# Performance work log

Hardware: AMD Instinct MI355X
Metric: run time of the kernel (lower is better)

## Reference

```python
import jax, jax.numpy as jnp
import numpy as np

C = 128      # channels
IN_A = 1024  # audio feature dim
IN_V = 512   # video feature dim
N = 20000    # nodes
E = 120000   # edges
NA = 10000   # number of audio nodes (placed first)
EPS = 1e-5


def _bn(h, p):
    # eval-mode BatchNorm1d: p = [gamma, beta, running_mean, running_var], each [F]
    return (h - p[2]) * jax.lax.rsqrt(p[3] + EPS) * p[0] + p[1]


def _lpp(h, bn1, W1, bn2, W2):
    # LinearPathPreact: BN -> ReLU -> Linear(no bias) -> BN -> ReLU -> Linear(no bias)
    h = jax.nn.relu(_bn(h, bn1)) @ W1.T
    h = jax.nn.relu(_bn(h, bn2)) @ W2.T
    return h


def _edge_conv(feats, src, dst, active, bn1, W1, bn2, W2, n_nodes):
    # PyG EdgeConv, aggr='max': out_i = max_{j->i} nn([x_i, x_j - x_i])
    xi = feats[dst]                      # [E, C] target features
    xj = feats[src]                      # [E, C] source features
    msg = _lpp(jnp.concatenate([xi, xj - xi], axis=-1), bn1, W1, bn2, W2)  # [E, C]
    neg = jnp.finfo(msg.dtype).min
    msg = jnp.where(active[:, None], msg, neg)  # mask out inactive edges for max
    agg = jax.ops.segment_max(msg, dst, num_segments=n_nodes)  # [N, C]
    return jnp.where(agg <= neg, jnp.zeros((), agg.dtype), agg)  # isolated nodes -> 0


def setup_inputs() -> dict:
    key = jax.random.key(0)
    ks = jax.random.split(key, 24)

    def bn_params(k, f, lead=()):
        kk = jax.random.split(k, 4)
        g = 1.0 + 0.1 * jax.random.normal(kk[0], lead + (f,), jnp.float32)
        b = 0.1 * jax.random.normal(kk[1], lead + (f,), jnp.float32)
        m = 0.1 * jax.random.normal(kk[2], lead + (f,), jnp.float32)
        v = 0.5 + jax.random.uniform(kk[3], lead + (f,), jnp.float32)
        return jnp.stack([g, b, m, v], axis=-2)  # lead + [4, f]

    inp = {}
    inp['x'] = jax.random.normal(ks[0], (N, 2, IN_A), jnp.float32)
    inp['edge_index'] = jax.random.randint(ks[1], (2, E), 0, N, dtype=jnp.int32)
    inp['edge_delta'] = jax.random.randint(ks[2], (E,), 0, 8, dtype=jnp.int32)
    inp['edge_self'] = jax.random.randint(ks[3], (E,), 0, 2, dtype=jnp.int32)
    inp['n_audio'] = NA

    s_a = (2.0 / IN_A) ** 0.5
    s_v = (2.0 / IN_V) ** 0.5
    s_2c = (2.0 / (2 * C)) ** 0.5
    s_c = (2.0 / C) ** 0.5
    inp['w0a'] = s_a * jax.random.normal(ks[4], (C, IN_A), jnp.float32)
    inp['b0a'] = 0.01 * jax.random.normal(ks[5], (C,), jnp.float32)
    inp['w0v'] = s_v * jax.random.normal(ks[6], (C, IN_V), jnp.float32)
    inp['b0v'] = 0.01 * jax.random.normal(ks[7], (C,), jnp.float32)
    inp['bn0'] = bn_params(ks[8], C)
    inp['bn_node'] = bn_params(ks[9], C, lead=(3,))          # batch_1..3: [3,4,C]
    # 8 EdgeConv MLPs in order [l1, l1t, l2, l2t, l3, l3t, l4, l4t]
    inp['ec_bn1'] = bn_params(ks[10], 2 * C, lead=(8,))      # [8,4,2C]
    inp['ec_fc1'] = s_2c * jax.random.normal(ks[11], (8, C, 2 * C), jnp.float32)
    inp['ec_bn2'] = bn_params(ks[12], C, lead=(8,))          # [8,4,C]
    inp['ec_fc2'] = s_c * jax.random.normal(ks[13], (8, C, C), jnp.float32)
    # heads: [fc, fc_a, fc_v]
    inp['w_heads'] = s_c * jax.random.normal(ks[14], (3, 2, C), jnp.float32)
    inp['b_heads'] = 0.01 * jax.random.normal(ks[15], (3, 2), jnp.float32)
    return inp


def reference(x, edge_index, edge_delta, edge_self, n_audio,
              w0a, b0a, w0v, b0v, bn0, bn_node,
              ec_bn1, ec_fc1, ec_bn2, ec_fc2, w_heads, b_heads):
    n = x.shape[0]
    src, dst = edge_index[0], edge_index[1]
    active1 = edge_delta < 1
    active2 = ((edge_delta >= 1) & (edge_delta < 4)) | (edge_self == 1)

    # layer 0: audio nodes are the first n_audio nodes (static split)
    a = x[:n_audio, 0, :IN_A] @ w0a.T + b0a          # [NA, C]
    v = x[n_audio:, 1, :IN_V] @ w0v.T + b0v          # [N-NA, C]
    g0 = jax.nn.relu(_bn(jnp.concatenate([a, v], axis=0), bn0))  # [N, C]

    def ec(f, k, act):
        return _edge_conv(f, src, dst, act, ec_bn1[k], ec_fc1[k], ec_bn2[k], ec_fc2[k], n)

    g1 = ec(ec(g0, 0, active1), 1, active2)
    g1 = jax.nn.relu(_bn(g1, bn_node[0]))            # dropout is identity (eval)
    g2 = ec(ec(g1, 2, active1), 3, active2) + g1
    g2 = jax.nn.relu(_bn(g2, bn_node[1]))
    g3 = ec(ec(g2, 4, active1), 5, active2) + g2
    g3 = jax.nn.relu(_bn(g3, bn_node[2]))
    g4 = ec(ec(g3, 6, active1), 7, active2) + g3

    out = g4 @ w_heads[0].T + b_heads[0]             # [N, 2]
    audio_out = g0[:n_audio] @ w_heads[1].T + b_heads[1]  # [NA, 2]
    video_out = g0[n_audio:] @ w_heads[2].T + b_heads[2]  # [N-NA, 2]
    return out, audio_out, video_out
```

## Files before the change

### kernel.cpp

```cpp
#include <hip/hip_runtime.h>

#define C 128
#define IN_A 1024
#define IN_V 512
#define NNODE 20000
#define NE 120000
#define NA 10000
#define NV 10000
#define EPSBN 1e-5f
#define NPAD 20032
#define EPAD 120064
#define NSTRIDE 20032

typedef __bf16 bf16_t;
typedef bf16_t bf16x8 __attribute__((ext_vector_type(8)));
typedef bf16_t bf16x2 __attribute__((ext_vector_type(2)));
typedef float f32x4 __attribute__((ext_vector_type(4)));
typedef unsigned int u32;

__device__ __forceinline__ f32x4 ld4(const float* p) {
    return *reinterpret_cast<const f32x4*>(p);
}
__device__ __forceinline__ f32x4 ld4nt(const float* p) {
    return __builtin_nontemporal_load(reinterpret_cast<const f32x4*>(p));
}
__device__ __forceinline__ int xcd_swz(int b, int n) {
    int q = n >> 3, r = n & 7;
    int x = b & 7, i = b >> 3;
    return (x < r ? x * (q + 1) : r * (q + 1) + (x - r) * q) + i;
}

struct PB {
    const float* x;
    const int* esrc; const int* edst; const int* edelta; const int* eself;
    const float* b0a; const float* b0v;
    const float* w0a; const float* w0v;
    const float* bn0; const float* bnn;
    const float* ecb1; const float* ecf1; const float* ecb2; const float* ecf2;
    const float* wh; const float* bh;
    float* out;
    bf16_t* W16; float* SBN; int* cnts; int* indeg; int* rowst; int* curs;
    int* psrc; int* pdst;
    float* U; bf16_t* G0; bf16_t* G1; bf16_t* msg;
};

__global__ void prep0(PB P) {
    int b = blockIdx.x, t = threadIdx.x;
    if (b < 2304) {
        int i = b * 256 + t;
        float v;
        if (i < 131072) v = P.w0a[i];
        else if (i < 196608) v = P.w0v[i - 131072];
        else if (i < 458752) v = P.ecf1[i - 196608];
        else v = P.ecf2[i - 458752];
        P.W16[i] = (bf16_t)v;
    } else if (b < 2318) {
        int i = (b - 2304) * 256 + t;
        if (i >= 28 * 128) return;
        int pair = i >> 7, cc = i & 127;
        float gg, bb, mm, vv;
        if (pair == 0)      { gg = P.bn0[cc]; bb = P.bn0[128 + cc]; mm = P.bn0[256 + cc]; vv = P.bn0[384 + cc]; }
        else if (pair < 4)  { const float* q = P.bnn + (pair - 1) * 512;
                              gg = q[cc]; bb = q[128 + cc]; mm = q[256 + cc]; vv = q[384 + cc]; }
        else if (pair < 12) { const float* q = P.ecb1 + (pair - 4) * 1024;
                              gg = q[cc]; bb = q[256 + cc]; mm = q[512 + cc]; vv = q[768 + cc]; }
        else if (pair < 20) { const float* q = P.ecb1 + (pair - 12) * 1024 + 128;
                              gg = q[cc]; bb = q[256 + cc]; mm = q[512 + cc]; vv = q[768 + cc]; }
        else                { const float* q = P.ecb2 + (pair - 20) * 512;
                              gg = q[cc]; bb = q[128 + cc]; mm = q[256 + cc]; vv = q[384 + cc]; }
        float sv = gg * rsqrtf(vv + EPSBN);
        P.SBN[pair * 256 + cc] = sv;
        P.SBN[pair * 256 + 128 + cc] = bb - mm * sv;
    } else {
        int e = (b - 2318) * 256 + t;
        if (e >= NE) return;
        int d = P.edelta[e];
        int dn = P.edst[e];
        if (d < 1) atomicAdd(P.indeg + dn, 1);
        if (((d >= 1) && (d < 4)) || (P.eself[e] == 1)) atomicAdd(P.indeg + NSTRIDE + dn, 1);
    }
}

__global__ __launch_bounds__(1024) void scan_kernel(PB P) {
    __shared__ int sh[1024];
    int half = blockIdx.x;
    const int* in = P.indeg + half * NSTRIDE;
    int* rsw = P.rowst + half * NSTRIDE;
    int* cu = P.curs + half * NSTRIDE;
    int t = threadIdx.x;
    int base = t * 20;
    int s = 0;
    for (int i = 0; i < 20; i++) { int idx = base + i; if (idx < NNODE) s += in[idx]; }
    sh[t] = s;
    __syncthreads();
    for (int off = 1; off < 1024; off <<= 1) {
        int v = (t >= off) ? sh[t - off] : 0;
        __syncthreads();
        sh[t] += v;
        __syncthreads();
    }
    int run = sh[t] - s;
    for (int i = 0; i < 20; i++) {
        int idx = base + i;
        if (idx < NNODE) { int v = in[idx]; rsw[idx] = run; cu[idx] = run; run += v; }
    }
    if (t == 1023) { rsw[NNODE] = sh[1023]; P.cnts[half] = sh[1023]; }
}

__global__ __launch_bounds__(256) void combo0(PB P) {
    __shared__ __align__(16) char smem[16384];
    int b = blockIdx.x;
    if (b >= 314) {
        int e = (b - 314) * 256 + threadIdx.x;
        if (e >= NE) return;
        int d = P.edelta[e];
        int dn = P.edst[e], sn = P.esrc[e];
        if (d < 1) {
            int q = atomicAdd(P.curs + dn, 1);
            P.psrc[q] = sn; P.pdst[q] = dn;
        }
        if (((d >= 1) && (d < 4)) || (P.eself[e] == 1)) {
            int q = atomicAdd(P.curs + NSTRIDE + dn, 1);
            P.psrc[EPAD + q] = sn; P.pdst[EPAD + q] = dn;
        }
        return;
    }
    int wave = threadIdx.x >> 6, lane = threadIdx.x & 63;
    bool audio = b < 157;
    int tile = audio ? b : b - 157;
    const float* A = audio ? P.x : P.x + (size_t)NA * 2048 + 1024;
    const bf16_t* W = audio ? P.W16 : P.W16 + 131072;
    const float* bias = audio ? P.b0a : P.b0v;
    int K = audio ? IN_A : IN_V;
    int M = audio ? NA : NV;
    int nbase = audio ? 0 : NA;
    int hsel = audio ? 1 : 2;

    int m0 = tile * 64 + wave * 16;
    int arow = m0 + (lane & 15);
    int ar = arow < M ? arow : (M - 1);
    int ak = (lane >> 4) << 3;
    const float* Af = A + (size_t)ar * 2048 + ak;
    const bf16_t* Bp = W + (size_t)(lane & 15) * K + ak;

    f32x4 acc[8];
#pragma unroll
    for (int i = 0; i < 8; i++) acc[i] = (f32x4)(0.0f);
    for (int kk = 0; kk < K; kk += 32) {
        f32x4 v0 = ld4nt(Af + kk), v1 = ld4nt(Af + kk + 4);
        bf16x8 a;
#pragma unroll
        for (int j = 0; j < 4; j++) { a[j] = (bf16_t)v0[j]; a[4 + j] = (bf16_t)v1[j]; }
#pragma unroll
        for (int nt = 0; nt < 8; nt++) {
            bf16x8 bb = *reinterpret_cast<const bf16x8*>(Bp + (size_t)nt * 16 * K + kk);
            acc[nt] = __builtin_amdgcn_mfma_f32_16x16x32_bf16(a, bb, acc[nt], 0, 0, 0);
        }
    }
    int cb = lane & 15;
    float se[8], he[8], bs[8], w0[8], w1[8], s1[8], t1[8];
#pragma unroll
    for (int nt = 0; nt < 8; nt++) {
        int n = nt * 16 + cb;
        se[nt] = P.SBN[n]; he[nt] = P.SBN[128 + n]; bs[nt] = bias[n];
        w0[nt] = P.wh[hsel * 256 + n]; w1[nt] = P.wh[hsel * 256 + 128 + n];
        s1[nt] = P.SBN[4 * 256 + n]; t1[nt] = P.SBN[4 * 256 + 128 + n];
    }
    int rbase = (lane >> 4) * 4;
#pragma unroll
    for (int j = 0; j < 4; j++) {
        int m = m0 + rbase + j;
        int r = wave * 16 + rbase + j;
        float hp0 = 0.f, hp1 = 0.f;
#pragma unroll
        for (int nt = 0; nt < 8; nt++) {
            int n = nt * 16 + cb;
            float v = fmaxf((acc[nt][j] + bs[nt]) * se[nt] + he[nt], 0.0f);
            if (m < M) P.G0[(size_t)(nbase + m) * C + n] = (bf16_t)v;
            hp0 += v * w0[nt]; hp1 += v * w1[nt];
            float av = fmaxf(v * s1[nt] + t1[nt], 0.0f);
            int byte = (r * 256 + 2 * n) ^ ((r & 7) << 4);
            *reinterpret_cast<bf16_t*>(smem + byte) = (bf16_t)av;
        }
#pragma unroll
        for (int o = 8; o; o >>= 1) { hp0 += __shfl_xor(hp0, o); hp1 += __shfl_xor(hp1, o); }
        if (cb == 0 && m < M) {
            float* op = audio ? (P.out + 40000 + (size_t)m * 2)
                              : (P.out + 60000 + (size_t)m * 2);
            op[0] = hp0 + P.bh[hsel * 2 + 0];
            op[1] = hp1 + P.bh[hsel * 2 + 1];
        }
    }
    const bf16_t* B2p = P.W16 + 196608 + (size_t)(lane & 15) * 256 + ak;
#pragma unroll
    for (int i = 0; i < 8; i++) acc[i] = (f32x4)(0.0f);
    int rr = wave * 16 + (lane & 15);
#pragma unroll
    for (int kk = 0; kk < C; kk += 32) {
        int byte = (rr * 256 + 2 * (ak + kk)) ^ ((rr & 7) << 4);
        bf16x8 a = *reinterpret_cast<const bf16x8*>(smem + byte);
#pragma unroll
        for (int nt = 0; nt < 8; nt++) {
            bf16x8 bb = *reinterpret_cast<const bf16x8*>(B2p + (size_t)nt * 16 * 256 + kk);
            acc[nt] = __builtin_amdgcn_mfma_f32_16x16x32_bf16(a, bb, acc[nt], 0, 0, 0);
        }
    }
#pragma unroll
    for (int j = 0; j < 4; j++) {
        int m = m0 + rbase + j;
        if (m >= M) continue;
#pragma unroll
        for (int nt = 0; nt < 8; nt++)
            P.U[(size_t)(nbase + m) * C + nt * 16 + cb] = acc[nt][j];
    }
}

__global__ __launch_bounds__(256) void edge_k(PB P, int h) {
    __shared__ __align__(16) float hlds[4 * 2048];
    int half = h & 1;
    int Mreal = P.cnts[half];
    int tiles = (Mreal + 63) >> 6;
    if ((int)blockIdx.x >= tiles) return;
    int m0b = xcd_swz(blockIdx.x, tiles) * 64;
    const bf16_t* F = half ? P.G1 : P.G0;
    const int* psrc = P.psrc + (half ? EPAD : 0);
    const int* pdst = P.pdst + (half ? EPAD : 0);
    const bf16_t* B1 = P.W16 + 196608 + (size_t)h * 32768 + 128;
    const bf16_t* B2 = P.W16 + 458752 + (size_t)h * 16384;
    const float* sA = P.SBN + (12 + h) * 256; const float* shA = sA + 128;
    const float* sE = P.SBN + (20 + h) * 256; const float* shE = sE + 128;

    int wave = threadIdx.x >> 6;
    int lane = threadIdx.x & 63;
    int m0 = m0b + wave * 16;
    int arow = m0 + (lane & 15);
    int ar = arow < Mreal ? arow : (Mreal - 1);
    int ak = (lane >> 4) << 3;

    const bf16_t* Fs = F + (size_t)psrc[ar] * C + ak;
    const bf16_t* Fd = F + (size_t)pdst[ar] * C + ak;
    const bf16_t* B1p = B1 + (size_t)(lane & 15) * 256 + ak;

    f32x4 acc[8];
#pragma unroll
    for (int i = 0; i < 8; i++) acc[i] = (f32x4)(0.0f);
#pragma unroll
    for (int kk = 0; kk < C; kk += 32) {
        bf16x8 s8 = *reinterpret_cast<const bf16x8*>(Fs + kk);
        bf16x8 d8 = *reinterpret_cast<const bf16x8*>(Fd + kk);
        f32x4 s0 = ld4(sA + kk + ak), s1 = ld4(sA + kk + ak + 4);
        f32x4 h0 = ld4(shA + kk + ak), h1 = ld4(shA + kk + ak + 4);
        bf16x8 a;
#pragma unroll
        for (int j = 0; j < 4; j++) {
            float t0 = fmaxf(((float)s8[j] - (float)d8[j]) * s0[j] + h0[j], 0.0f);
            float t1 = fmaxf(((float)s8[4 + j] - (float)d8[4 + j]) * s1[j] + h1[j], 0.0f);
            a[j] = (bf16_t)t0; a[4 + j] = (bf16_t)t1;
        }
#pragma unroll
        for (int nt = 0; nt < 8; nt++) {
            bf16x8 bb = *reinterpret_cast<const bf16x8*>(B1p + (size_t)nt * 16 * 256 + kk);
            acc[nt] = __builtin_amdgcn_mfma_f32_16x16x32_bf16(a, bb, acc[nt], 0, 0, 0);
        }
    }
    int cb = lane & 15;
    float se[8], he[8];
#pragma unroll
    for (int nt = 0; nt < 8; nt++) { se[nt] = sE[nt * 16 + cb]; he[nt] = shE[nt * 16 + cb]; }
    int rbase = (lane >> 4) * 4;
    float* wl = hlds + wave * 2048;
#pragma unroll
    for (int j = 0; j < 4; j++) {
        int m = m0 + rbase + j;
        int mc = m < Mreal ? m : (Mreal - 1);
        const float* Ur = P.U + (size_t)pdst[mc] * C;
        int r = rbase + j;
        int sw = (r & 7) << 2;
#pragma unroll
        for (int nt = 0; nt < 8; nt++) {
            int n = nt * 16 + cb;
            float v = acc[nt][j] + Ur[n];
            wl[(r * 128 + n) ^ sw] = fmaxf(v * se[nt] + he[nt], 0.0f);
        }
    }
    const bf16_t* B2p = B2 + (size_t)(lane & 15) * C + ak;
#pragma unroll
    for (int i = 0; i < 8; i++) acc[i] = (f32x4)(0.0f);
    int rr = lane & 15;
    int swz = (rr & 7) << 2;
    const float* rl = hlds + wave * 2048;
#pragma unroll
    for (int kk = 0; kk < C; kk += 32) {
        int c0 = kk + ak;
        f32x4 v0 = *reinterpret_cast<const f32x4*>(rl + ((rr * 128 + c0) ^ swz));
        f32x4 v1 = *reinterpret_cast<const f32x4*>(rl + ((rr * 128 + c0 + 4) ^ swz));
        bf16x8 a;
#pragma unroll
        for (int j = 0; j < 4; j++) { a[j] = (bf16_t)v0[j]; a[4 + j] = (bf16_t)v1[j]; }
#pragma unroll
        for (int nt = 0; nt < 8; nt++) {
            bf16x8 bb = *reinterpret_cast<const bf16x8*>(B2p + (size_t)nt * 16 * C + kk);
            acc[nt] = __builtin_amdgcn_mfma_f32_16x16x32_bf16(a, bb, acc[nt], 0, 0, 0);
        }
    }
#pragma unroll
    for (int j = 0; j < 4; j++) {
        int m = m0 + rbase + j;
        if (m < Mreal) {
            bf16_t* op = P.msg + (size_t)m * C;
#pragma unroll
            for (int nt = 0; nt < 8; nt++) op[nt * 16 + cb] = (bf16_t)acc[nt][j];
        }
    }
}

__global__ __launch_bounds__(512) void aggk1(PB P, int h) {
    __shared__ __align__(16) char smem[4096];
    int half = h & 1, p = h >> 1;
    int tile = xcd_swz(blockIdx.x, 1250);
    int wave = threadIdx.x >> 6;
    int lane = threadIdx.x & 63;
    const int* rs = P.rowst + half * NSTRIDE;
    const u32* msgu = (const u32*)P.msg;
    int c = lane * 2;

    const float* s1a = P.SBN + (5 + h) * 256;
    float s1c0 = s1a[c], s1c1 = s1a[c + 1], h1c0 = s1a[128 + c], h1c1 = s1a[128 + c + 1];
    float sn0 = 0.f, sn1 = 0.f, hn0 = 0.f, hn1 = 0.f;
    if (half && p < 3) {
        const float* q = P.SBN + (1 + p) * 256;
        sn0 = q[c]; sn1 = q[c + 1]; hn0 = q[128 + c]; hn1 = q[128 + c + 1];
    }
    float w0c0 = 0.f, w0c1 = 0.f, w1c0 = 0.f, w1c1 = 0.f;
    if (h == 7) { w0c0 = P.wh[c]; w0c1 = P.wh[c + 1]; w1c0 = P.wh[128 + c]; w1c1 = P.wh[129 + c]; }

#pragma unroll
    for (int i = 0; i < 2; i++) {
        int n = tile * 16 + wave * 2 + i;
        int r = wave * 2 + i;
        float a0 = 0.f, a1 = 0.f;
        if (n < NNODE) {
            int p0 = rs[n], p1 = rs[n + 1];
            float v0 = -INFINITY, v1 = -INFINITY;
            int q = p0;
            for (; q + 1 < p1; q += 2) {
                u32 u0 = msgu[(size_t)q * 64 + lane];
                u32 u1 = msgu[(size_t)(q + 1) * 64 + lane];
                v0 = fmaxf(v0, __uint_as_float(u0 << 16));
                v1 = fmaxf(v1, __uint_as_float(u0 & 0xffff0000u));
                v0 = fmaxf(v0, __uint_as_float(u1 << 16));
                v1 = fmaxf(v1, __uint_as_float(u1 & 0xffff0000u));
            }
            if (q < p1) {
                u32 u = msgu[(size_t)q * 64 + lane];
                v0 = fmaxf(v0, __uint_as_float(u << 16));
                v1 = fmaxf(v1, __uint_as_float(u & 0xffff0000u));
            }
            if (p1 == p0) { v0 = 0.f; v1 = 0.f; }
            if (h == 7) {
                bf16x2 r2 = *((const bf16x2*)(P.G0 + (size_t)n * C) + lane);
                v0 += (float)r2[0]; v1 += (float)r2[1];
                float q0 = v0 * w0c0 + v1 * w0c1;
                float q1 = v0 * w1c0 + v1 * w1c1;
#pragma unroll
                for (int o = 32; o; o >>= 1) { q0 += __shfl_down(q0, o); q1 += __shfl_down(q1, o); }
                if (lane == 0) {
                    P.out[(size_t)n * 2 + 0] = q0 + P.bh[0];
                    P.out[(size_t)n * 2 + 1] = q1 + P.bh[1];
                }
            } else {
                float g0v, g1v;
                if (!half) {
                    g0v = v0; g1v = v1;
                    bf16x2 w; w[0] = (bf16_t)g0v; w[1] = (bf16_t)g1v;
                    *((bf16x2*)(P.G1 + (size_t)n * C) + lane) = w;
                } else {
                    float r0 = 0.f, r1 = 0.f;
                    if (p >= 1) {
                        bf16x2 r2 = *((const bf16x2*)(P.G0 + (size_t)n * C) + lane);
                        r0 = (float)r2[0]; r1 = (float)r2[1];
                    }
                    g0v = fmaxf((v0 + r0) * sn0 + hn0, 0.0f);
                    g1v = fmaxf((v1 + r1) * sn1 + hn1, 0.0f);
                    bf16x2 w; w[0] = (bf16_t)g0v; w[1] = (bf16_t)g1v;
                    *((bf16x2*)(P.G0 + (size_t)n * C) + lane) = w;
                }
                a0 = fmaxf(g0v * s1c0 + h1c0, 0.0f);
                a1 = fmaxf(g1v * s1c1 + h1c1, 0.0f);
            }
        }
        if (h < 7) {
            int byte = (r * 256 + lane * 4) ^ ((r & 7) << 4);
            bf16x2 t; t[0] = (bf16_t)a0; t[1] = (bf16_t)a1;
            *reinterpret_cast<bf16x2*>(smem + byte) = t;
        }
    }
    if (h == 7) return;
    __syncthreads();
    const bf16_t* B = P.W16 + 196608 + (size_t)(h + 1) * 32768;
    int cb = lane & 15;
    int ak = (lane >> 4) << 3;
    const bf16_t* Bp = B + (size_t)(wave * 16 + cb) * 256 + ak;
    f32x4 acc = (f32x4)(0.0f);
#pragma unroll
    for (int kk = 0; kk < C; kk += 32) {
        int byte = (cb * 256 + 2 * (ak + kk)) ^ ((cb & 7) << 4);
        bf16x8 a = *reinterpret_cast<const bf16x8*>(smem + byte);
        bf16x8 bb = *reinterpret_cast<const bf16x8*>(Bp + kk);
        acc = __builtin_amdgcn_mfma_f32_16x16x32_bf16(a, bb, acc, 0, 0, 0);
    }
#pragma unroll
    for (int j = 0; j < 4; j++) {
        int m = tile * 16 + (lane >> 4) * 4 + j;
        if (m < NNODE) P.U[(size_t)m * C + wave * 16 + cb] = acc[j];
    }
}

extern "C" void kernel_launch(void* const* d_in, const int* in_sizes, int n_in,
                              void* d_out, int out_size, void* d_ws, size_t ws_size,
                              hipStream_t stream) {
    PB P;
    P.x      = (const float*)d_in[0];
    const int* eidx = (const int*)d_in[1];
    P.esrc   = eidx;
    P.edst   = eidx + NE;
    P.edelta = (const int*)d_in[2];
    P.eself  = (const int*)d_in[3];
    P.w0a    = (const float*)d_in[5];
    P.b0a    = (const float*)d_in[6];
    P.w0v    = (const float*)d_in[7];
    P.b0v    = (const float*)d_in[8];
    P.bn0    = (const float*)d_in[9];
    P.bnn    = (const float*)d_in[10];
    P.ecb1   = (const float*)d_in[11];
    P.ecf1   = (const float*)d_in[12];
    P.ecb2   = (const float*)d_in[13];
    P.ecf2   = (const float*)d_in[14];
    P.wh     = (const float*)d_in[15];
    P.bh     = (const float*)d_in[16];
    P.out    = (float*)d_out;

    char* wsb = (char*)d_ws;
    size_t off = 0;
    auto take = [&](size_t bytes) -> char* {
        char* p = wsb + off;
        off = (off + bytes + 255) & ~(size_t)255;
        return p;
    };
    P.W16   = (bf16_t*)take(589824 * 2);
    P.SBN   = (float*)take(28 * 256 * 4);
    P.cnts  = (int*)take(256);
    P.indeg = (int*)take(2 * NSTRIDE * 4);
    P.rowst = (int*)take((2 * NSTRIDE + 64) * 4);
    P.curs  = (int*)take(2 * NSTRIDE * 4);
    P.psrc  = (int*)take(2 * (size_t)EPAD * 4);
    P.pdst  = (int*)take(2 * (size_t)EPAD * 4);
    P.U     = (float*)take((size_t)NPAD * C * 4);
    P.G0    = (bf16_t*)take((size_t)NPAD * C * 2);
    P.G1    = (bf16_t*)take((size_t)NPAD * C * 2);
    P.msg   = (bf16_t*)take((size_t)EPAD * C * 2);
    (void)ws_size; (void)in_sizes; (void)n_in; (void)out_size;

    hipMemsetAsync(P.indeg, 0, 2 * NSTRIDE * 4, stream);
    prep0<<<2787, 256, 0, stream>>>(P);
    scan_kernel<<<2, 1024, 0, stream>>>(P);
    combo0<<<783, 256, 0, stream>>>(P);
    for (int h = 0; h < 8; h++) {
        edge_k<<<EPAD / 64, 256, 0, stream>>>(P, h);
        aggk1<<<1250, 512, 0, stream>>>(P, h);
    }
}
```

Measured before the change: 524.2 us.

## Compute x_i half of first EdgeConv linear per edge instead of precomputed node table

Removes the per-node precomputation U = W1a·relu(bn(x_i)) that combo0 and aggk1 produced, along with its fp32 workspace buffer. Instead edge_k now runs a full K=256 MFMA per edge: the destination-feature half (BN and ReLU on x_i) and the difference half (x_j - x_i). This drops the per-node GEMMs and the random fp32 U gathers per edge, at the cost of doubling the first-layer MFMA work in the edge kernel. It also adds an occupancy hint of 4 blocks per CU on edge_k.

```diff
diff --git a/kernel.cpp b/kernel.cpp
--- a/kernel.cpp
+++ b/kernel.cpp
@@ -41,7 +41,7 @@
     float* out;
     bf16_t* W16; float* SBN; int* cnts; int* indeg; int* rowst; int* curs;
     int* psrc; int* pdst;
-    float* U; bf16_t* G0; bf16_t* G1; bf16_t* msg;
+    bf16_t* G0; bf16_t* G1; bf16_t* msg;
 };
 
 __global__ void prep0(PB P) {
@@ -108,7 +108,6 @@
 }
 
 __global__ __launch_bounds__(256) void combo0(PB P) {
-    __shared__ __align__(16) char smem[16384];
     int b = blockIdx.x;
     if (b >= 314) {
         int e = (b - 314) * 256 + threadIdx.x;
@@ -158,19 +157,17 @@
         }
     }
     int cb = lane & 15;
-    float se[8], he[8], bs[8], w0[8], w1[8], s1[8], t1[8];
+    float se[8], he[8], bs[8], w0[8], w1[8];
 #pragma unroll
     for (int nt = 0; nt < 8; nt++) {
         int n = nt * 16 + cb;
         se[nt] = P.SBN[n]; he[nt] = P.SBN[128 + n]; bs[nt] = bias[n];
         w0[nt] = P.wh[hsel * 256 + n]; w1[nt] = P.wh[hsel * 256 + 128 + n];
-        s1[nt] = P.SBN[4 * 256 + n]; t1[nt] = P.SBN[4 * 256 + 128 + n];
     }
     int rbase = (lane >> 4) * 4;
 #pragma unroll
     for (int j = 0; j < 4; j++) {
         int m = m0 + rbase + j;
-        int r = wave * 16 + rbase + j;
         float hp0 = 0.f, hp1 = 0.f;
 #pragma unroll
         for (int nt = 0; nt < 8; nt++) {
@@ -178,9 +175,6 @@
             float v = fmaxf((acc[nt][j] + bs[nt]) * se[nt] + he[nt], 0.0f);
             if (m < M) P.G0[(size_t)(nbase + m) * C + n] = (bf16_t)v;
             hp0 += v * w0[nt]; hp1 += v * w1[nt];
-            float av = fmaxf(v * s1[nt] + t1[nt], 0.0f);
-            int byte = (r * 256 + 2 * n) ^ ((r & 7) << 4);
-            *reinterpret_cast<bf16_t*>(smem + byte) = (bf16_t)av;
         }
 #pragma unroll
         for (int o = 8; o; o >>= 1) { hp0 += __shfl_xor(hp0, o); hp1 += __shfl_xor(hp1, o); }
@@ -191,31 +185,9 @@
             op[1] = hp1 + P.bh[hsel * 2 + 1];
         }
     }
-    const bf16_t* B2p = P.W16 + 196608 + (size_t)(lane & 15) * 256 + ak;
-#pragma unroll
-    for (int i = 0; i < 8; i++) acc[i] = (f32x4)(0.0f);
-    int rr = wave * 16 + (lane & 15);
-#pragma unroll
-    for (int kk = 0; kk < C; kk += 32) {
-        int byte = (rr * 256 + 2 * (ak + kk)) ^ ((rr & 7) << 4);
-        bf16x8 a = *reinterpret_cast<const bf16x8*>(smem + byte);
-#pragma unroll
-        for (int nt = 0; nt < 8; nt++) {
-            bf16x8 bb = *reinterpret_cast<const bf16x8*>(B2p + (size_t)nt * 16 * 256 + kk);
-            acc[nt] = __builtin_amdgcn_mfma_f32_16x16x32_bf16(a, bb, acc[nt], 0, 0, 0);
-        }
-    }
-#pragma unroll
-    for (int j = 0; j < 4; j++) {
-        int m = m0 + rbase + j;
-        if (m >= M) continue;
-#pragma unroll
-        for (int nt = 0; nt < 8; nt++)
-            P.U[(size_t)(nbase + m) * C + nt * 16 + cb] = acc[nt][j];
-    }
-}
-
-__global__ __launch_bounds__(256) void edge_k(PB P, int h) {
+}
+
+__global__ __launch_bounds__(256, 4) void edge_k(PB P, int h) {
     __shared__ __align__(16) float hlds[4 * 2048];
     int half = h & 1;
     int Mreal = P.cnts[half];
@@ -225,9 +197,10 @@
     const bf16_t* F = half ? P.G1 : P.G0;
     const int* psrc = P.psrc + (half ? EPAD : 0);
     const int* pdst = P.pdst + (half ? EPAD : 0);
-    const bf16_t* B1 = P.W16 + 196608 + (size_t)h * 32768 + 128;
+    const bf16_t* B1 = P.W16 + 196608 + (size_t)h * 32768;
     const bf16_t* B2 = P.W16 + 458752 + (size_t)h * 16384;
-    const float* sA = P.SBN + (12 + h) * 256; const float* shA = sA + 128;
+    const float* sA1 = P.SBN + (4 + h) * 256;
+    const float* sA2 = P.SBN + (12 + h) * 256;
     const float* sE = P.SBN + (20 + h) * 256; const float* shE = sE + 128;
 
     int wave = threadIdx.x >> 6;
@@ -244,18 +217,21 @@
     f32x4 acc[8];
 #pragma unroll
     for (int i = 0; i < 8; i++) acc[i] = (f32x4)(0.0f);
-#pragma unroll
-    for (int kk = 0; kk < C; kk += 32) {
-        bf16x8 s8 = *reinterpret_cast<const bf16x8*>(Fs + kk);
-        bf16x8 d8 = *reinterpret_cast<const bf16x8*>(Fd + kk);
-        f32x4 s0 = ld4(sA + kk + ak), s1 = ld4(sA + kk + ak + 4);
-        f32x4 h0 = ld4(shA + kk + ak), h1 = ld4(shA + kk + ak + 4);
+
+    bf16x8 fd[4];
+#pragma unroll
+    for (int q = 0; q < 4; q++) fd[q] = *reinterpret_cast<const bf16x8*>(Fd + q * 32);
+
+#pragma unroll
+    for (int q = 0; q < 4; q++) {
+        int kk = q * 32;
+        f32x4 s0 = ld4(sA1 + kk + ak), s1 = ld4(sA1 + kk + ak + 4);
+        f32x4 h0 = ld4(sA1 + 128 + kk + ak), h1 = ld4(sA1 + 128 + kk + ak + 4);
         bf16x8 a;
 #pragma unroll
         for (int j = 0; j < 4; j++) {
-            float t0 = fmaxf(((float)s8[j] - (float)d8[j]) * s0[j] + h0[j], 0.0f);
-            float t1 = fmaxf(((float)s8[4 + j] - (float)d8[4 + j]) * s1[j] + h1[j], 0.0f);
-            a[j] = (bf16_t)t0; a[4 + j] = (bf16_t)t1;
+            a[j]     = (bf16_t)fmaxf((float)fd[q][j] * s0[j] + h0[j], 0.0f);
+            a[4 + j] = (bf16_t)fmaxf((float)fd[q][4 + j] * s1[j] + h1[j], 0.0f);
         }
 #pragma unroll
         for (int nt = 0; nt < 8; nt++) {
@@ -263,6 +239,25 @@
             acc[nt] = __builtin_amdgcn_mfma_f32_16x16x32_bf16(a, bb, acc[nt], 0, 0, 0);
         }
     }
+#pragma unroll
+    for (int q = 0; q < 4; q++) {
+        int kk = q * 32;
+        bf16x8 s8 = *reinterpret_cast<const bf16x8*>(Fs + kk);
+        f32x4 s0 = ld4(sA2 + kk + ak), s1 = ld4(sA2 + kk + ak + 4);
+        f32x4 h0 = ld4(sA2 + 128 + kk + ak), h1 = ld4(sA2 + 128 + kk + ak + 4);
+        bf16x8 a;
+#pragma unroll
+        for (int j = 0; j < 4; j++) {
+            a[j]     = (bf16_t)fmaxf(((float)s8[j] - (float)fd[q][j]) * s0[j] + h0[j], 0.0f);
+            a[4 + j] = (bf16_t)fmaxf(((float)s8[4 + j] - (float)fd[q][4 + j]) * s1[j] + h1[j], 0.0f);
+        }
+#pragma unroll
+        for (int nt = 0; nt < 8; nt++) {
+            bf16x8 bb = *reinterpret_cast<const bf16x8*>(B1p + (size_t)nt * 16 * 256 + 128 + kk);
+            acc[nt] = __builtin_amdgcn_mfma_f32_16x16x32_bf16(a, bb, acc[nt], 0, 0, 0);
+        }
+    }
+
     int cb = lane & 15;
     float se[8], he[8];
 #pragma unroll
@@ -271,16 +266,12 @@
     float* wl = hlds + wave * 2048;
 #pragma unroll
     for (int j = 0; j < 4; j++) {
-        int m = m0 + rbase + j;
-        int mc = m < Mreal ? m : (Mreal - 1);
-        const float* Ur = P.U + (size_t)pdst[mc] * C;
         int r = rbase + j;
         int sw = (r & 7) << 2;
 #pragma unroll
         for (int nt = 0; nt < 8; nt++) {
             int n = nt * 16 + cb;
-            float v = acc[nt][j] + Ur[n];
-            wl[(r * 128 + n) ^ sw] = fmaxf(v * se[nt] + he[nt], 0.0f);
+            wl[(r * 128 + n) ^ sw] = fmaxf(acc[nt][j] * se[nt] + he[nt], 0.0f);
         }
     }
     const bf16_t* B2p = B2 + (size_t)(lane & 15) * C + ak;
@@ -315,7 +306,6 @@
 }
 
 __global__ __launch_bounds__(512) void aggk1(PB P, int h) {
-    __shared__ __align__(16) char smem[4096];
     int half = h & 1, p = h >> 1;
     int tile = xcd_swz(blockIdx.x, 1250);
     int wave = threadIdx.x >> 6;
@@ -324,8 +314,6 @@
     const u32* msgu = (const u32*)P.msg;
     int c = lane * 2;
 
-    const float* s1a = P.SBN + (5 + h) * 256;
-    float s1c0 = s1a[c], s1c1 = s1a[c + 1], h1c0 = s1a[128 + c], h1c1 = s1a[128 + c + 1];
     float sn0 = 0.f, sn1 = 0.f, hn0 = 0.f, hn1 = 0.f;
     if (half && p < 3) {
         const float* q = P.SBN + (1 + p) * 256;
@@ -337,82 +325,49 @@
 #pragma unroll
     for (int i = 0; i < 2; i++) {
         int n = tile * 16 + wave * 2 + i;
-        int r = wave * 2 + i;
-        float a0 = 0.f, a1 = 0.f;
-        if (n < NNODE) {
-            int p0 = rs[n], p1 = rs[n + 1];
-            float v0 = -INFINITY, v1 = -INFINITY;
-            int q = p0;
-            for (; q + 1 < p1; q += 2) {
-                u32 u0 = msgu[(size_t)q * 64 + lane];
-                u32 u1 = msgu[(size_t)(q + 1) * 64 + lane];
-                v0 = fmaxf(v0, __uint_as_float(u0 << 16));
-                v1 = fmaxf(v1, __uint_as_float(u0 & 0xffff0000u));
-                v0 = fmaxf(v0, __uint_as_float(u1 << 16));
-                v1 = fmaxf(v1, __uint_as_float(u1 & 0xffff0000u));
+        if (n >= NNODE) continue;
+        int p0 = rs[n], p1 = rs[n + 1];
+        float v0 = -INFINITY, v1 = -INFINITY;
+        int q = p0;
+        for (; q + 1 < p1; q += 2) {
+            u32 u0 = msgu[(size_t)q * 64 + lane];
+            u32 u1 = msgu[(size_t)(q + 1) * 64 + lane];
+            v0 = fmaxf(v0, __uint_as_float(u0 << 16));
+            v1 = fmaxf(v1, __uint_as_float(u0 & 0xffff0000u));
+            v0 = fmaxf(v0, __uint_as_float(u1 << 16));
+            v1 = fmaxf(v1, __uint_as_float(u1 & 0xffff0000u));
+        }
+        if (q < p1) {
+            u32 u = msgu[(size_t)q * 64 + lane];
+            v0 = fmaxf(v0, __uint_as_float(u << 16));
+            v1 = fmaxf(v1, __uint_as_float(u & 0xffff0000u));
+        }
+        if (p1 == p0) { v0 = 0.f; v1 = 0.f; }
+        if (h == 7) {
+            bf16x2 r2 = *((const bf16x2*)(P.G0 + (size_t)n * C) + lane);
+            v0 += (float)r2[0]; v1 += (float)r2[1];
+            float q0 = v0 * w0c0 + v1 * w0c1;
+            float q1 = v0 * w1c0 + v1 * w1c1;
+#pragma unroll
+            for (int o = 32; o; o >>= 1) { q0 += __shfl_down(q0, o); q1 += __shfl_down(q1, o); }
+            if (lane == 0) {
+                P.out[(size_t)n * 2 + 0] = q0 + P.bh[0];
+                P.out[(size_t)n * 2 + 1] = q1 + P.bh[1];
             }
-            if (q < p1) {
-                u32 u = msgu[(size_t)q * 64 + lane];
-                v0 = fmaxf(v0, __uint_as_float(u << 16));
-                v1 = fmaxf(v1, __uint_as_float(u & 0xffff0000u));
+        } else if (!half) {
+            bf16x2 w; w[0] = (bf16_t)v0; w[1] = (bf16_t)v1;
+            *((bf16x2*)(P.G1 + (size_t)n * C) + lane) = w;
+        } else {
+            float r0 = 0.f, r1 = 0.f;
+            if (p >= 1) {
+                bf16x2 r2 = *((const bf16x2*)(P.G0 + (size_t)n * C) + lane);
+                r0 = (float)r2[0]; r1 = (float)r2[1];
             }
-            if (p1 == p0) { v0 = 0.f; v1 = 0.f; }
-            if (h == 7) {
-                bf16x2 r2 = *((const bf16x2*)(P.G0 + (size_t)n * C) + lane);
-                v0 += (float)r2[0]; v1 += (float)r2[1];
-                float q0 = v0 * w0c0 + v1 * w0c1;
-                float q1 = v0 * w1c0 + v1 * w1c1;
-#pragma unroll
-                for (int o = 32; o; o >>= 1) { q0 += __shfl_down(q0, o); q1 += __shfl_down(q1, o); }
-                if (lane == 0) {
-                    P.out[(size_t)n * 2 + 0] = q0 + P.bh[0];
-                    P.out[(size_t)n * 2 + 1] = q1 + P.bh[1];
-                }
-            } else {
-                float g0v, g1v;
-                if (!half) {
-                    g0v = v0; g1v = v1;
-                    bf16x2 w; w[0] = (bf16_t)g0v; w[1] = (bf16_t)g1v;
-                    *((bf16x2*)(P.G1 + (size_t)n * C) + lane) = w;
-                } else {
-                    float r0 = 0.f, r1 = 0.f;
-                    if (p >= 1) {
-                        bf16x2 r2 = *((const bf16x2*)(P.G0 + (size_t)n * C) + lane);
-                        r0 = (float)r2[0]; r1 = (float)r2[1];
-                    }
-                    g0v = fmaxf((v0 + r0) * sn0 + hn0, 0.0f);
-                    g1v = fmaxf((v1 + r1) * sn1 + hn1, 0.0f);
-                    bf16x2 w; w[0] = (bf16_t)g0v; w[1] = (bf16_t)g1v;
-                    *((bf16x2*)(P.G0 + (size_t)n * C) + lane) = w;
-                }
-                a0 = fmaxf(g0v * s1c0 + h1c0, 0.0f);
-                a1 = fmaxf(g1v * s1c1 + h1c1, 0.0f);
-            }
-        }
-        if (h < 7) {
-            int byte = (r * 256 + lane * 4) ^ ((r & 7) << 4);
-            bf16x2 t; t[0] = (bf16_t)a0; t[1] = (bf16_t)a1;
-            *reinterpret_cast<bf16x2*>(smem + byte) = t;
-        }
-    }
-    if (h == 7) return;
-    __syncthreads();
-    const bf16_t* B = P.W16 + 196608 + (size_t)(h + 1) * 32768;
-    int cb = lane & 15;
-    int ak = (lane >> 4) << 3;
-    const bf16_t* Bp = B + (size_t)(wave * 16 + cb) * 256 + ak;
-    f32x4 acc = (f32x4)(0.0f);
-#pragma unroll
-    for (int kk = 0; kk < C; kk += 32) {
-        int byte = (cb * 256 + 2 * (ak + kk)) ^ ((cb & 7) << 4);
-        bf16x8 a = *reinterpret_cast<const bf16x8*>(smem + byte);
-        bf16x8 bb = *reinterpret_cast<const bf16x8*>(Bp + kk);
-        acc = __builtin_amdgcn_mfma_f32_16x16x32_bf16(a, bb, acc, 0, 0, 0);
-    }
-#pragma unroll
-    for (int j = 0; j < 4; j++) {
-        int m = tile * 16 + (lane >> 4) * 4 + j;
-        if (m < NNODE) P.U[(size_t)m * C + wave * 16 + cb] = acc[j];
+            float g0v = fmaxf((v0 + r0) * sn0 + hn0, 0.0f);
+            float g1v = fmaxf((v1 + r1) * sn1 + hn1, 0.0f);
+            bf16x2 w; w[0] = (bf16_t)g0v; w[1] = (bf16_t)g1v;
+            *((bf16x2*)(P.G0 + (size_t)n * C) + lane) = w;
+        }
     }
 }
 
@@ -455,7 +410,6 @@
     P.curs  = (int*)take(2 * NSTRIDE * 4);
     P.psrc  = (int*)take(2 * (size_t)EPAD * 4);
     P.pdst  = (int*)take(2 * (size_t)EPAD * 4);
-    P.U     = (float*)take((size_t)NPAD * C * 4);
     P.G0    = (bf16_t*)take((size_t)NPAD * C * 2);
     P.G1    = (bf16_t*)take((size_t)NPAD * C * 2);
     P.msg   = (bf16_t*)take((size_t)EPAD * C * 2);
```

Result: slower. 592.0 us (+12.9%).

## Split edge MLP into two column passes with bf16 LDS staging for occupancy

Applied to the files above, without the earlier changes.

The edge kernel now computes each 128-column GEMM in two 64-column passes with four accumulators instead of eight. It precomputes the BN/ReLU input fragments once and reuses them across passes. The hidden activations are staged in LDS as bf16 rather than fp32, which halves shared memory per block. A min-blocks launch bound of 5 asks the compiler to cap registers for higher occupancy. In exchange, the edge input fragments stay live across both passes and the BN scale/shift are reloaded per element, which may cause spills under the register cap.

```diff
diff --git a/kernel.cpp b/kernel.cpp
--- a/kernel.cpp
+++ b/kernel.cpp
@@ -215,8 +215,8 @@
     }
 }
 
-__global__ __launch_bounds__(256) void edge_k(PB P, int h) {
-    __shared__ __align__(16) float hlds[4 * 2048];
+__global__ __launch_bounds__(256, 5) void edge_k(PB P, int h) {
+    __shared__ __align__(16) char hb[4][4096];
     int half = h & 1;
     int Mreal = P.cnts[half];
     int tiles = (Mreal + 63) >> 6;
@@ -236,80 +236,100 @@
     int arow = m0 + (lane & 15);
     int ar = arow < Mreal ? arow : (Mreal - 1);
     int ak = (lane >> 4) << 3;
+    int cb = lane & 15;
+    int rbase = (lane >> 4) * 4;
 
     const bf16_t* Fs = F + (size_t)psrc[ar] * C + ak;
     const bf16_t* Fd = F + (size_t)pdst[ar] * C + ak;
-    const bf16_t* B1p = B1 + (size_t)(lane & 15) * 256 + ak;
-
-    f32x4 acc[8];
-#pragma unroll
-    for (int i = 0; i < 8; i++) acc[i] = (f32x4)(0.0f);
-#pragma unroll
-    for (int kk = 0; kk < C; kk += 32) {
-        bf16x8 s8 = *reinterpret_cast<const bf16x8*>(Fs + kk);
-        bf16x8 d8 = *reinterpret_cast<const bf16x8*>(Fd + kk);
-        f32x4 s0 = ld4(sA + kk + ak), s1 = ld4(sA + kk + ak + 4);
-        f32x4 h0 = ld4(shA + kk + ak), h1 = ld4(shA + kk + ak + 4);
-        bf16x8 a;
-#pragma unroll
-        for (int j = 0; j < 4; j++) {
-            float t0 = fmaxf(((float)s8[j] - (float)d8[j]) * s0[j] + h0[j], 0.0f);
-            float t1 = fmaxf(((float)s8[4 + j] - (float)d8[4 + j]) * s1[j] + h1[j], 0.0f);
-            a[j] = (bf16_t)t0; a[4 + j] = (bf16_t)t1;
-        }
-#pragma unroll
-        for (int nt = 0; nt < 8; nt++) {
-            bf16x8 bb = *reinterpret_cast<const bf16x8*>(B1p + (size_t)nt * 16 * 256 + kk);
-            acc[nt] = __builtin_amdgcn_mfma_f32_16x16x32_bf16(a, bb, acc[nt], 0, 0, 0);
-        }
-    }
-    int cb = lane & 15;
-    float se[8], he[8];
-#pragma unroll
-    for (int nt = 0; nt < 8; nt++) { se[nt] = sE[nt * 16 + cb]; he[nt] = shE[nt * 16 + cb]; }
-    int rbase = (lane >> 4) * 4;
-    float* wl = hlds + wave * 2048;
+
+    int dj[4];
 #pragma unroll
     for (int j = 0; j < 4; j++) {
         int m = m0 + rbase + j;
-        int mc = m < Mreal ? m : (Mreal - 1);
-        const float* Ur = P.U + (size_t)pdst[mc] * C;
-        int r = rbase + j;
-        int sw = (r & 7) << 2;
-#pragma unroll
-        for (int nt = 0; nt < 8; nt++) {
-            int n = nt * 16 + cb;
-            float v = acc[nt][j] + Ur[n];
-            wl[(r * 128 + n) ^ sw] = fmaxf(v * se[nt] + he[nt], 0.0f);
-        }
-    }
-    const bf16_t* B2p = B2 + (size_t)(lane & 15) * C + ak;
-#pragma unroll
-    for (int i = 0; i < 8; i++) acc[i] = (f32x4)(0.0f);
+        dj[j] = pdst[m < Mreal ? m : (Mreal - 1)];
+    }
+
+    bf16x8 av[4];
+    {
+        bf16x8 fs[4], fdv[4];
+#pragma unroll
+        for (int q = 0; q < 4; q++) {
+            fs[q]  = *reinterpret_cast<const bf16x8*>(Fs + q * 32);
+            fdv[q] = *reinterpret_cast<const bf16x8*>(Fd + q * 32);
+        }
+#pragma unroll
+        for (int q = 0; q < 4; q++) {
+            int kk = q * 32;
+            f32x4 s0 = ld4(sA + kk + ak), s1 = ld4(sA + kk + ak + 4);
+            f32x4 h0 = ld4(shA + kk + ak), h1 = ld4(shA + kk + ak + 4);
+            bf16x8 a;
+#pragma unroll
+            for (int j = 0; j < 4; j++) {
+                a[j]     = (bf16_t)fmaxf(((float)fs[q][j] - (float)fdv[q][j]) * s0[j] + h0[j], 0.0f);
+                a[4 + j] = (bf16_t)fmaxf(((float)fs[q][4 + j] - (float)fdv[q][4 + j]) * s1[j] + h1[j], 0.0f);
+            }
+            av[q] = a;
+        }
+    }
+
+    char* wl = hb[wave];
+
+#pragma unroll
+    for (int pass = 0; pass < 2; pass++) {
+        f32x4 acc[4];
+#pragma unroll
+        for (int i = 0; i < 4; i++) acc[i] = (f32x4)(0.0f);
+#pragma unroll
+        for (int q = 0; q < 4; q++) {
+            int kk = q * 32;
+#pragma unroll
+            for (int nt = 0; nt < 4; nt++) {
+                const bf16_t* bp = B1 + (size_t)((pass * 4 + nt) * 16 + cb) * 256 + kk + ak;
+                bf16x8 bb = *reinterpret_cast<const bf16x8*>(bp);
+                acc[nt] = __builtin_amdgcn_mfma_f32_16x16x32_bf16(av[q], bb, acc[nt], 0, 0, 0);
+            }
+        }
+#pragma unroll
+        for (int j = 0; j < 4; j++) {
+            const float* Ur = P.U + (size_t)dj[j] * C + pass * 64;
+            int r = rbase + j;
+#pragma unroll
+            for (int nt = 0; nt < 4; nt++) {
+                int n = nt * 16 + cb;
+                int gn = pass * 64 + n;
+                float v = acc[nt][j] + Ur[n];
+                float hv = fmaxf(v * sE[gn] + shE[gn], 0.0f);
+                int byte = (r * 256 + 2 * gn) ^ ((r & 7) << 4);
+                *reinterpret_cast<bf16_t*>(wl + byte) = (bf16_t)hv;
+            }
+        }
+    }
     int rr = lane & 15;
-    int swz = (rr & 7) << 2;
-    const float* rl = hlds + wave * 2048;
-#pragma unroll
-    for (int kk = 0; kk < C; kk += 32) {
-        int c0 = kk + ak;
-        f32x4 v0 = *reinterpret_cast<const f32x4*>(rl + ((rr * 128 + c0) ^ swz));
-        f32x4 v1 = *reinterpret_cast<const f32x4*>(rl + ((rr * 128 + c0 + 4) ^ swz));
-        bf16x8 a;
-#pragma unroll
-        for (int j = 0; j < 4; j++) { a[j] = (bf16_t)v0[j]; a[4 + j] = (bf16_t)v1[j]; }
-#pragma unroll
-        for (int nt = 0; nt < 8; nt++) {
-            bf16x8 bb = *reinterpret_cast<const bf16x8*>(B2p + (size_t)nt * 16 * C + kk);
-            acc[nt] = __builtin_amdgcn_mfma_f32_16x16x32_bf16(a, bb, acc[nt], 0, 0, 0);
-        }
-    }
-#pragma unroll
-    for (int j = 0; j < 4; j++) {
-        int m = m0 + rbase + j;
-        if (m < Mreal) {
-            bf16_t* op = P.msg + (size_t)m * C;
-#pragma unroll
-            for (int nt = 0; nt < 8; nt++) op[nt * 16 + cb] = (bf16_t)acc[nt][j];
+#pragma unroll
+    for (int pass = 0; pass < 2; pass++) {
+        f32x4 acc[4];
+#pragma unroll
+        for (int i = 0; i < 4; i++) acc[i] = (f32x4)(0.0f);
+#pragma unroll
+        for (int q = 0; q < 4; q++) {
+            int kk = q * 32;
+            int byte = (rr * 256 + 2 * (kk + ak)) ^ ((rr & 7) << 4);
+            bf16x8 a = *reinterpret_cast<const bf16x8*>(wl + byte);
+#pragma unroll
+            for (int nt = 0; nt < 4; nt++) {
+                const bf16_t* bp = B2 + (size_t)((pass * 4 + nt) * 16 + cb) * C + kk + ak;
+                bf16x8 bb = *reinterpret_cast<const bf16x8*>(bp);
+                acc[nt] = __builtin_amdgcn_mfma_f32_16x16x32_bf16(a, bb, acc[nt], 0, 0, 0);
+            }
+        }
+#pragma unroll
+        for (int j = 0; j < 4; j++) {
+            int m = m0 + rbase + j;
+            if (m < Mreal) {
+                bf16_t* op = P.msg + (size_t)m * C + pass * 64;
+#pragma unroll
+                for (int nt = 0; nt < 4; nt++) op[nt * 16 + cb] = (bf16_t)acc[nt][j];
+            }
         }
     }
 }
```

Result: slower. 543.8 us (+3.8%).
